# Kernel optimization log

Hardware: AMD Instinct MI355X
Metric: run time of the kernel (lower is better)

The kernel has to match this reference:

```python
import jax, jax.numpy as jnp
import numpy as np

N = 100_000   # nodes
E = 1_600_000 # edges
F = 32        # input features
G = 512       # graphs in batch
EPS = 1e-5    # batchnorm eps


def setup_inputs() -> dict:
    key = jax.random.key(0)
    ks = jax.random.split(key, 24)
    d = {
        "x": jax.random.normal(ks[0], (N, F), jnp.float32),
        "edge_index": jax.random.randint(ks[1], (2, E), 0, N),
        "batch": jnp.sort(jax.random.randint(ks[2], (N,), 0, G)),
        "Wl1": jax.random.normal(ks[3], (30, F), jnp.float32) * 0.1,
        "bl1": jax.random.normal(ks[4], (30,), jnp.float32) * 0.1,
        "Wr1": jax.random.normal(ks[5], (30, F), jnp.float32) * 0.1,
        "Wl2": jax.random.normal(ks[6], (30, 30), jnp.float32) * 0.1,
        "bl2": jax.random.normal(ks[7], (30,), jnp.float32) * 0.1,
        "Wr2": jax.random.normal(ks[8], (30, 30), jnp.float32) * 0.1,
        "g1": jax.random.uniform(ks[9], (30,), jnp.float32) + 0.5,
        "b1": jax.random.normal(ks[10], (30,), jnp.float32) * 0.1,
        "m1": jax.random.normal(ks[11], (30,), jnp.float32) * 0.1,
        "v1": jax.random.uniform(ks[12], (30,), jnp.float32) + 0.5,
        "g2": jax.random.uniform(ks[13], (30,), jnp.float32) + 0.5,
        "b2": jax.random.normal(ks[14], (30,), jnp.float32) * 0.1,
        "m2": jax.random.normal(ks[15], (30,), jnp.float32) * 0.1,
        "v2": jax.random.uniform(ks[16], (30,), jnp.float32) + 0.5,
        "W1": jax.random.normal(ks[17], (10, 60), jnp.float32) * 0.1,
        "bb1": jax.random.normal(ks[18], (10,), jnp.float32) * 0.1,
        "W2": jax.random.normal(ks[19], (1, 10), jnp.float32) * 0.1,
        "bb2": jax.random.normal(ks[20], (1,), jnp.float32) * 0.1,
    }
    return d


def reference(x, edge_index, batch, Wl1, bl1, Wr1, Wl2, bl2, Wr2,
              g1, b1, m1, v1, g2, b2, m2, v2, W1, bb1, W2, bb2):
    src, dst = edge_index[0], edge_index[1]

    def sage(h, Wl, bl, Wr):
        # mean aggregation of source features into targets (PyG SAGEConv default)
        s = jax.ops.segment_sum(h[src], dst, num_segments=N)
        cnt = jax.ops.segment_sum(jnp.ones((E,), h.dtype), dst, num_segments=N)
        agg = s / jnp.maximum(cnt, 1.0)[:, None]
        return agg @ Wl.T + bl + h @ Wr.T

    def bn(h, g, b, m, v):  # BatchNorm1d, eval mode (running stats)
        return (h - m) * jax.lax.rsqrt(v + EPS) * g + b

    h = bn(jax.nn.relu(sage(x, Wl1, bl1, Wr1)), g1, b1, m1, v1)
    h = bn(jax.nn.relu(sage(h, Wl2, bl2, Wr2)), g2, b2, m2, v2)

    # dual segment pooling over graphs
    xmax = jax.ops.segment_max(h, batch, num_segments=G)
    xmax = jnp.where(jnp.isfinite(xmax), xmax, 0.0)  # empty graphs -> 0
    s = jax.ops.segment_sum(h, batch, num_segments=G)
    c = jax.ops.segment_sum(jnp.ones((N,), h.dtype), batch, num_segments=G)
    xmean = s / jnp.maximum(c, 1.0)[:, None]

    z = jnp.concatenate([xmax, xmean], axis=1)  # [G, 60]
    z = jax.nn.relu(z @ W1.T + bb1)
    z = z @ W2.T + bb2
    return jax.nn.sigmoid(z)  # [G, 1]
```

## Files before the change

kernel.cpp:

```cpp
#include <hip/hip_runtime.h>
#include <hip/hip_fp16.h>

#define NN 100000
#define NE 1600000
#define FI 32
#define FH 30
#define PAD 32
#define NG 512
#define NBK 782
#define BNODES 128
#define SCB 1024
#define CBLK 32
#define NCHUNK (SCB / CBLK)
#define CAP 4096
#define NB1 391
#define THB 6250

__global__ __launch_bounds__(256) void k_phist(const int* __restrict__ dst, int* __restrict__ partial,
                                               const float* __restrict__ x, __half2* __restrict__ xh)
{
    __shared__ int cnt[NBK];
    if (blockIdx.x >= SCB) {
        int i = (blockIdx.x - SCB) * 256 + threadIdx.x;
        if (i < NN * (PAD / 2)) {
            float2 f = ((const float2*)x)[i];
            xh[i] = __floats2half2_rn(f.x, f.y);
        }
        return;
    }
    for (int i = threadIdx.x; i < NBK; i += 256) cnt[i] = 0;
    __syncthreads();
    for (int e = blockIdx.x * 256 + threadIdx.x; e < NE; e += SCB * 256)
        atomicAdd(&cnt[dst[e] >> 7], 1);
    __syncthreads();
    for (int i = threadIdx.x; i < NBK; i += 256)
        partial[(size_t)blockIdx.x * NBK + i] = cnt[i];
}

__global__ __launch_bounds__(256) void k_csum(const int* __restrict__ partial, int* __restrict__ chunksum)
{
    int t = blockIdx.x * 256 + threadIdx.x;
    if (t >= NCHUNK * NBK) return;
    int c = t / NBK, b = t - c * NBK;
    int s = 0;
    #pragma unroll 8
    for (int k = 0; k < CBLK; ++k)
        s += partial[(size_t)(c * CBLK + k) * NBK + b];
    chunksum[c * NBK + b] = s;
}

__global__ __launch_bounds__(1024) void k_cscan(const int* __restrict__ chunksum,
                                                int* __restrict__ chunkbase, int* __restrict__ bktOff)
{
    __shared__ int tmp[1024];
    int tid = threadIdx.x;
    int cs[NCHUNK];
    int total = 0;
    if (tid < NBK) {
        #pragma unroll
        for (int c = 0; c < NCHUNK; ++c) { cs[c] = chunksum[c * NBK + tid]; total += cs[c]; }
    }
    tmp[tid] = (tid < NBK) ? total : 0;
    __syncthreads();
    for (int off = 1; off < 1024; off <<= 1) {
        int t = (tid >= off) ? tmp[tid - off] : 0;
        __syncthreads();
        tmp[tid] += t;
        __syncthreads();
    }
    if (tid < NBK) {
        int run = tmp[tid] - total;
        bktOff[tid] = run;
        #pragma unroll
        for (int c = 0; c < NCHUNK; ++c) { chunkbase[c * NBK + tid] = run; run += cs[c]; }
    }
    if (tid == 0) bktOff[NBK] = NE;
}

__global__ __launch_bounds__(256) void k_base(int* __restrict__ partial, const int* __restrict__ chunkbase)
{
    int t = blockIdx.x * 256 + threadIdx.x;
    if (t >= NCHUNK * NBK) return;
    int c = t / NBK, b = t - c * NBK;
    int run = chunkbase[c * NBK + b];
    #pragma unroll 8
    for (int k = 0; k < CBLK; ++k) {
        size_t idx = (size_t)(c * CBLK + k) * NBK + b;
        int v = partial[idx];
        partial[idx] = run;
        run += v;
    }
}

__global__ __launch_bounds__(256) void k_bscat(const int* __restrict__ src, const int* __restrict__ dst,
                                               const int* __restrict__ partial, unsigned* __restrict__ pairs)
{
    __shared__ int sbase[NBK];
    __shared__ int scnt[NBK];
    for (int i = threadIdx.x; i < NBK; i += 256) {
        sbase[i] = partial[(size_t)blockIdx.x * NBK + i];
        scnt[i] = 0;
    }
    __syncthreads();
    for (int e = blockIdx.x * 256 + threadIdx.x; e < NE; e += SCB * 256) {
        int d = dst[e];
        int b = d >> 7;
        int r = atomicAdd(&scnt[b], 1);
        pairs[sbase[b] + r] = ((unsigned)src[e] << 7) | (unsigned)(d & 127);
    }
}

__global__ __launch_bounds__(256) void k_csr(
    const int* __restrict__ bktOff, const unsigned* __restrict__ pairs,
    int* __restrict__ rowstart, int* __restrict__ col)
{
    __shared__ unsigned sp[CAP];
    __shared__ int bins[BNODES], binpos[BNODES], stmp[BNODES];
    int tid = threadIdx.x;
    int bkt = blockIdx.x;
    int gbase = bktOff[bkt];
    int cnt = bktOff[bkt + 1] - gbase;
    if (tid < BNODES) bins[tid] = 0;
    __syncthreads();
    bool inl = (cnt <= CAP);
    if (inl) {
        for (int i = tid; i < cnt; i += 256) {
            unsigned u = pairs[gbase + i];
            sp[i] = u;
            atomicAdd(&bins[u & 127], 1);
        }
    } else {
        for (int i = tid; i < cnt; i += 256)
            atomicAdd(&bins[pairs[gbase + i] & 127], 1);
    }
    __syncthreads();
    if (tid < BNODES) stmp[tid] = bins[tid];
    __syncthreads();
    for (int off = 1; off < BNODES; off <<= 1) {
        int t = 0;
        if (tid < BNODES && tid >= off) t = stmp[tid - off];
        __syncthreads();
        if (tid < BNODES) stmp[tid] += t;
        __syncthreads();
    }
    if (tid < BNODES) {
        int ex = stmp[tid] - bins[tid];
        binpos[tid] = ex;
        int n = (bkt << 7) + tid;
        if (n < NN) rowstart[n] = gbase + ex;
        if (bkt == 0 && tid == 0) rowstart[NN] = NE;
    }
    __syncthreads();
    if (inl) {
        for (int i = tid; i < cnt; i += 256) {
            unsigned u = sp[i];
            int p = atomicAdd(&binpos[u & 127], 1);
            col[gbase + p] = (int)(u >> 7);
        }
    } else {
        for (int i = tid; i < cnt; i += 256) {
            unsigned u = pairs[gbase + i];
            int p = atomicAdd(&binpos[u & 127], 1);
            col[gbase + p] = (int)(u >> 7);
        }
    }
}

__global__ __launch_bounds__(256) void k_aggcsr_h(const int* __restrict__ rowstart,
                                                  const int* __restrict__ col,
                                                  const uint4* __restrict__ hin,
                                                  float* __restrict__ aggout)
{
    int tid = blockIdx.x * 256 + threadIdx.x;
    int n = tid >> 6;
    if (n >= NN) return;
    int lane = threadIdx.x & 63;
    int q = lane & 3;
    int grp = lane >> 2;
    int rs = rowstart[n], re = rowstart[n + 1];
    float a0 = 0.0f, a1 = 0.0f, a2 = 0.0f, a3 = 0.0f;
    float a4 = 0.0f, a5 = 0.0f, a6 = 0.0f, a7 = 0.0f;
    for (int e = rs + grp; e < re; e += 16) {
        uint4 u = hin[(size_t)col[e] * 4 + q];
        float2 f0 = __half22float2(*(const __half2*)&u.x);
        float2 f1 = __half22float2(*(const __half2*)&u.y);
        float2 f2 = __half22float2(*(const __half2*)&u.z);
        float2 f3 = __half22float2(*(const __half2*)&u.w);
        a0 += f0.x; a1 += f0.y; a2 += f1.x; a3 += f1.y;
        a4 += f2.x; a5 += f2.y; a6 += f3.x; a7 += f3.y;
    }
    #pragma unroll
    for (int off = 4; off < 64; off <<= 1) {
        a0 += __shfl_xor(a0, off); a1 += __shfl_xor(a1, off);
        a2 += __shfl_xor(a2, off); a3 += __shfl_xor(a3, off);
        a4 += __shfl_xor(a4, off); a5 += __shfl_xor(a5, off);
        a6 += __shfl_xor(a6, off); a7 += __shfl_xor(a7, off);
    }
    if (lane < 4) {
        float inv = (re > rs) ? 1.0f / (float)(re - rs) : 0.0f;
        float4* o = (float4*)(aggout + (size_t)n * PAD + q * 8);
        o[0] = make_float4(a0 * inv, a1 * inv, a2 * inv, a3 * inv);
        o[1] = make_float4(a4 * inv, a5 * inv, a6 * inv, a7 * inv);
    }
}

__global__ __launch_bounds__(256) void k_t1(
    const float* __restrict__ x, const float* __restrict__ agg,
    const float* __restrict__ Wl, const float* __restrict__ bl, const float* __restrict__ Wr,
    const float* __restrict__ g, const float* __restrict__ b,
    const float* __restrict__ m, const float* __restrict__ v,
    __half2* __restrict__ h1h)
{
    __shared__ float sWl[FH * FI], sWr[FH * FI], sBias[FH], sScale[FH], sShift[FH];
    for (int i = threadIdx.x; i < FH * FI; i += 256) { sWl[i] = Wl[i]; sWr[i] = Wr[i]; }
    if (threadIdx.x < FH) {
        int j = threadIdx.x;
        float sc = g[j] * rsqrtf(v[j] + 1e-5f);
        sBias[j] = bl[j];
        sScale[j] = sc;
        sShift[j] = b[j] - m[j] * sc;
    }
    __syncthreads();
    int n = blockIdx.x * 256 + threadIdx.x;
    if (n >= NN) return;
    float xr[FI], ar[FI];
    #pragma unroll
    for (int k = 0; k < FI; k += 4) {
        float4 xv = *(const float4*)(x + (size_t)n * FI + k);
        float4 av = *(const float4*)(agg + (size_t)n * PAD + k);
        xr[k] = xv.x; xr[k+1] = xv.y; xr[k+2] = xv.z; xr[k+3] = xv.w;
        ar[k] = av.x; ar[k+1] = av.y; ar[k+2] = av.z; ar[k+3] = av.w;
    }
    float res[FH];
    for (int j = 0; j < FH; ++j) {
        float acc = sBias[j];
        #pragma unroll
        for (int k = 0; k < FI; ++k)
            acc += ar[k] * sWl[j * FI + k] + xr[k] * sWr[j * FI + k];
        acc = fmaxf(acc, 0.0f);
        res[j] = acc * sScale[j] + sShift[j];
    }
    __half2* row = h1h + (size_t)n * (PAD / 2);
    #pragma unroll
    for (int j = 0; j < FH; j += 2)
        row[j >> 1] = __floats2half2_rn(res[j], res[j + 1]);
    row[15] = __floats2half2_rn(0.0f, 0.0f);
}

__global__ __launch_bounds__(256) void k_t2(
    const __half2* __restrict__ h1h, const float* __restrict__ agg,
    const float* __restrict__ Wl, const float* __restrict__ bl, const float* __restrict__ Wr,
    const float* __restrict__ g, const float* __restrict__ b,
    const float* __restrict__ m, const float* __restrict__ v,
    __half2* __restrict__ h2h)
{
    __shared__ float sWl[FH * FH], sWr[FH * FH], sBias[FH], sScale[FH], sShift[FH];
    for (int i = threadIdx.x; i < FH * FH; i += 256) { sWl[i] = Wl[i]; sWr[i] = Wr[i]; }
    if (threadIdx.x < FH) {
        int j = threadIdx.x;
        float sc = g[j] * rsqrtf(v[j] + 1e-5f);
        sBias[j] = bl[j];
        sScale[j] = sc;
        sShift[j] = b[j] - m[j] * sc;
    }
    __syncthreads();
    int n = blockIdx.x * 256 + threadIdx.x;
    if (n >= NN) return;
    float xr[FH], ar[FH];
    const __half2* hrow = h1h + (size_t)n * (PAD / 2);
    #pragma unroll
    for (int k2 = 0; k2 < FH / 2; ++k2) {
        float2 fv = __half22float2(hrow[k2]);
        xr[2 * k2] = fv.x; xr[2 * k2 + 1] = fv.y;
    }
    #pragma unroll
    for (int k = 0; k < FH; ++k)
        ar[k] = agg[(size_t)n * PAD + k];
    float res[FH];
    for (int j = 0; j < FH; ++j) {
        float acc = sBias[j];
        #pragma unroll
        for (int k = 0; k < FH; ++k)
            acc += ar[k] * sWl[j * FH + k] + xr[k] * sWr[j * FH + k];
        acc = fmaxf(acc, 0.0f);
        res[j] = acc * sScale[j] + sShift[j];
    }
    __half2* row = h2h + (size_t)n * (PAD / 2);
    #pragma unroll
    for (int j = 0; j < FH; j += 2)
        row[j >> 1] = __floats2half2_rn(res[j], res[j + 1]);
    row[15] = __floats2half2_rn(0.0f, 0.0f);
}

__global__ __launch_bounds__(256) void k_pool(
    const __half* __restrict__ h2, const int* __restrict__ batch,
    const float* __restrict__ W1, const float* __restrict__ bb1,
    const float* __restrict__ W2, const float* __restrict__ bb2,
    float* __restrict__ out)
{
    __shared__ float sS[8][FH], sM[8][FH], sz[2 * FH], st[10];
    int tid = threadIdx.x;
    int gi = blockIdx.x;
    int lo = 0, hi = NN;
    while (lo < hi) { int mid = (lo + hi) >> 1; if (batch[mid] < gi) lo = mid + 1; else hi = mid; }
    int start = lo;
    hi = NN;
    while (lo < hi) { int mid = (lo + hi) >> 1; if (batch[mid] <= gi) lo = mid + 1; else hi = mid; }
    int end = lo;

    int f = tid & 31;
    int ng = tid >> 5;
    float sum = 0.0f, mx = -INFINITY;
    if (f < FH) {
        for (int n = start + ng; n < end; n += 8) {
            float val = __half2float(h2[(size_t)n * PAD + f]);
            sum += val;
            mx = fmaxf(mx, val);
        }
        sS[ng][f] = sum;
        sM[ng][f] = mx;
    }
    __syncthreads();
    if (tid < FH) {
        float s = 0.0f, mm = -INFINITY;
        #pragma unroll
        for (int w = 0; w < 8; ++w) { s += sS[w][tid]; mm = fmaxf(mm, sM[w][tid]); }
        int c = end - start;
        sz[tid]      = (c > 0) ? mm : 0.0f;
        sz[FH + tid] = (c > 0) ? s / (float)c : 0.0f;
    }
    __syncthreads();
    if (tid < 10) {
        float t = bb1[tid];
        for (int k = 0; k < 2 * FH; ++k) t += sz[k] * W1[tid * 2 * FH + k];
        st[tid] = fmaxf(t, 0.0f);
    }
    __syncthreads();
    if (tid == 0) {
        float o = bb2[0];
        for (int j = 0; j < 10; ++j) o += st[j] * W2[j];
        out[gi] = 1.0f / (1.0f + expf(-o));
    }
}

extern "C" void kernel_launch(void* const* d_in, const int* in_sizes, int n_in,
                              void* d_out, int out_size, void* d_ws, size_t ws_size,
                              hipStream_t stream)
{
    const float* x   = (const float*)d_in[0];
    const int*   ei  = (const int*)d_in[1];
    const int*   bat = (const int*)d_in[2];
    const float* Wl1 = (const float*)d_in[3];
    const float* bl1 = (const float*)d_in[4];
    const float* Wr1 = (const float*)d_in[5];
    const float* Wl2 = (const float*)d_in[6];
    const float* bl2 = (const float*)d_in[7];
    const float* Wr2 = (const float*)d_in[8];
    const float* g1  = (const float*)d_in[9];
    const float* b1  = (const float*)d_in[10];
    const float* m1  = (const float*)d_in[11];
    const float* v1  = (const float*)d_in[12];
    const float* g2  = (const float*)d_in[13];
    const float* b2  = (const float*)d_in[14];
    const float* m2  = (const float*)d_in[15];
    const float* v2  = (const float*)d_in[16];
    const float* W1  = (const float*)d_in[17];
    const float* bb1 = (const float*)d_in[18];
    const float* W2  = (const float*)d_in[19];
    const float* bb2 = (const float*)d_in[20];

    const int* src = ei;
    const int* dst = ei + NE;

    int* wsi = (int*)d_ws;
    int*      partial   = wsi;
    int*      chunksum  = partial + (size_t)SCB * NBK;
    int*      chunkbase = chunksum + NCHUNK * NBK;
    int*      bktOff    = chunkbase + NCHUNK * NBK;
    int*      rowstart  = bktOff + NBK + 2;
    unsigned* pairs     = (unsigned*)(rowstart + NN + 4);
    int*      col       = (int*)(pairs + NE);
    __half2*  xh        = (__half2*)(col + NE);
    __half2*  h1h       = xh + (size_t)NN * (PAD / 2);
    __half2*  h2h       = h1h + (size_t)NN * (PAD / 2);
    float*    aggbuf    = (float*)(h2h + (size_t)NN * (PAD / 2));

    int pb = (NCHUNK * NBK + 255) / 256;

    k_phist <<<SCB + THB, 256, 0, stream>>>(dst, partial, x, xh);
    k_csum  <<<pb, 256, 0, stream>>>(partial, chunksum);
    k_cscan <<<1, 1024, 0, stream>>>(chunksum, chunkbase, bktOff);
    k_base  <<<pb, 256, 0, stream>>>(partial, chunkbase);
    k_bscat <<<SCB, 256, 0, stream>>>(src, dst, partial, pairs);
    k_csr   <<<NBK, 256, 0, stream>>>(bktOff, pairs, rowstart, col);

    int ab = (NN * 64 + 255) / 256;
    k_aggcsr_h<<<ab, 256, 0, stream>>>(rowstart, col, (const uint4*)xh, aggbuf);
    k_t1<<<NB1, 256, 0, stream>>>(x, aggbuf, Wl1, bl1, Wr1, g1, b1, m1, v1, h1h);
    k_aggcsr_h<<<ab, 256, 0, stream>>>(rowstart, col, (const uint4*)h1h, aggbuf);
    k_t2<<<NB1, 256, 0, stream>>>(h1h, aggbuf, Wl2, bl2, Wr2, g2, b2, m2, v2, h2h);
    k_pool<<<NG, 256, 0, stream>>>((const __half*)h2h, bat, W1, bb1, W2, bb2, (float*)d_out);
}
```

Measured before the change: 193.4 us.

## Gather node features in FP8 and shrink histogram partials to 16-bit

Node features for both aggregation passes are now stored as packed FP8 (32 bytes per row), so each gathered row is two 16-byte loads instead of four. Each wavefront processes 32 edges per iteration instead of 16, and the aggregation kernel is rewritten around this layout. Separately, the per-block bucket histogram partials become 16-bit, holding only offsets within a bucket, with the global bucket offset added in the scatter kernel; this halves the scan traffic. FP8 storage loses a lot of precision on x and h1 and risks exceeding the accuracy tolerance.

```diff
diff --git a/kernel.cpp b/kernel.cpp
--- a/kernel.cpp
+++ b/kernel.cpp
@@ -14,17 +14,21 @@
 #define NCHUNK (SCB / CBLK)
 #define CAP 4096
 #define NB1 391
-#define THB 6250
-
-__global__ __launch_bounds__(256) void k_phist(const int* __restrict__ dst, int* __restrict__ partial,
-                                               const float* __restrict__ x, __half2* __restrict__ xh)
+#define F8B 3125
+
+__global__ __launch_bounds__(256) void k_phist(const int* __restrict__ dst,
+                                               unsigned short* __restrict__ partial,
+                                               const float* __restrict__ x, unsigned* __restrict__ x8)
 {
     __shared__ int cnt[NBK];
     if (blockIdx.x >= SCB) {
         int i = (blockIdx.x - SCB) * 256 + threadIdx.x;
-        if (i < NN * (PAD / 2)) {
-            float2 f = ((const float2*)x)[i];
-            xh[i] = __floats2half2_rn(f.x, f.y);
+        if (i < NN * 8) {
+            float4 f = ((const float4*)x)[i];
+            unsigned w = 0;
+            w = __builtin_amdgcn_cvt_pk_fp8_f32(f.x, f.y, w, false);
+            w = __builtin_amdgcn_cvt_pk_fp8_f32(f.z, f.w, w, true);
+            x8[i] = w;
         }
         return;
     }
@@ -34,10 +38,11 @@
         atomicAdd(&cnt[dst[e] >> 7], 1);
     __syncthreads();
     for (int i = threadIdx.x; i < NBK; i += 256)
-        partial[(size_t)blockIdx.x * NBK + i] = cnt[i];
-}
-
-__global__ __launch_bounds__(256) void k_csum(const int* __restrict__ partial, int* __restrict__ chunksum)
+        partial[(size_t)blockIdx.x * NBK + i] = (unsigned short)cnt[i];
+}
+
+__global__ __launch_bounds__(256) void k_csum(const unsigned short* __restrict__ partial,
+                                              int* __restrict__ chunksum)
 {
     int t = blockIdx.x * 256 + threadIdx.x;
     if (t >= NCHUNK * NBK) return;
@@ -69,15 +74,16 @@
         __syncthreads();
     }
     if (tid < NBK) {
-        int run = tmp[tid] - total;
-        bktOff[tid] = run;
+        bktOff[tid] = tmp[tid] - total;
+        int run = 0;
         #pragma unroll
         for (int c = 0; c < NCHUNK; ++c) { chunkbase[c * NBK + tid] = run; run += cs[c]; }
     }
     if (tid == 0) bktOff[NBK] = NE;
 }
 
-__global__ __launch_bounds__(256) void k_base(int* __restrict__ partial, const int* __restrict__ chunkbase)
+__global__ __launch_bounds__(256) void k_base(unsigned short* __restrict__ partial,
+                                              const int* __restrict__ chunkbase)
 {
     int t = blockIdx.x * 256 + threadIdx.x;
     if (t >= NCHUNK * NBK) return;
@@ -87,18 +93,20 @@
     for (int k = 0; k < CBLK; ++k) {
         size_t idx = (size_t)(c * CBLK + k) * NBK + b;
         int v = partial[idx];
-        partial[idx] = run;
+        partial[idx] = (unsigned short)run;
         run += v;
     }
 }
 
 __global__ __launch_bounds__(256) void k_bscat(const int* __restrict__ src, const int* __restrict__ dst,
-                                               const int* __restrict__ partial, unsigned* __restrict__ pairs)
+                                               const unsigned short* __restrict__ partial,
+                                               const int* __restrict__ bktOff,
+                                               unsigned* __restrict__ pairs)
 {
     __shared__ int sbase[NBK];
     __shared__ int scnt[NBK];
     for (int i = threadIdx.x; i < NBK; i += 256) {
-        sbase[i] = partial[(size_t)blockIdx.x * NBK + i];
+        sbase[i] = bktOff[i] + (int)partial[(size_t)blockIdx.x * NBK + i];
         scnt[i] = 0;
     }
     __syncthreads();
@@ -166,41 +174,48 @@
     }
 }
 
-__global__ __launch_bounds__(256) void k_aggcsr_h(const int* __restrict__ rowstart,
-                                                  const int* __restrict__ col,
-                                                  const uint4* __restrict__ hin,
-                                                  float* __restrict__ aggout)
+__global__ __launch_bounds__(256) void k_agg8(const int* __restrict__ rowstart,
+                                              const int* __restrict__ col,
+                                              const uint4* __restrict__ hin,
+                                              float* __restrict__ aggout)
 {
     int tid = blockIdx.x * 256 + threadIdx.x;
     int n = tid >> 6;
     if (n >= NN) return;
     int lane = threadIdx.x & 63;
-    int q = lane & 3;
-    int grp = lane >> 2;
+    int q = lane & 1;
+    int grp = lane >> 1;
     int rs = rowstart[n], re = rowstart[n + 1];
-    float a0 = 0.0f, a1 = 0.0f, a2 = 0.0f, a3 = 0.0f;
-    float a4 = 0.0f, a5 = 0.0f, a6 = 0.0f, a7 = 0.0f;
-    for (int e = rs + grp; e < re; e += 16) {
-        uint4 u = hin[(size_t)col[e] * 4 + q];
-        float2 f0 = __half22float2(*(const __half2*)&u.x);
-        float2 f1 = __half22float2(*(const __half2*)&u.y);
-        float2 f2 = __half22float2(*(const __half2*)&u.z);
-        float2 f3 = __half22float2(*(const __half2*)&u.w);
-        a0 += f0.x; a1 += f0.y; a2 += f1.x; a3 += f1.y;
-        a4 += f2.x; a5 += f2.y; a6 += f3.x; a7 += f3.y;
-    }
-    #pragma unroll
-    for (int off = 4; off < 64; off <<= 1) {
-        a0 += __shfl_xor(a0, off); a1 += __shfl_xor(a1, off);
-        a2 += __shfl_xor(a2, off); a3 += __shfl_xor(a3, off);
-        a4 += __shfl_xor(a4, off); a5 += __shfl_xor(a5, off);
-        a6 += __shfl_xor(a6, off); a7 += __shfl_xor(a7, off);
-    }
-    if (lane < 4) {
+    float a[16];
+    #pragma unroll
+    for (int i = 0; i < 16; ++i) a[i] = 0.0f;
+    for (int e = rs + grp; e < re; e += 32) {
+        uint4 u = hin[(size_t)col[e] * 2 + q];
+        auto f0 = __builtin_amdgcn_cvt_pk_f32_fp8(u.x, false);
+        auto f1 = __builtin_amdgcn_cvt_pk_f32_fp8(u.x, true);
+        auto f2 = __builtin_amdgcn_cvt_pk_f32_fp8(u.y, false);
+        auto f3 = __builtin_amdgcn_cvt_pk_f32_fp8(u.y, true);
+        auto f4 = __builtin_amdgcn_cvt_pk_f32_fp8(u.z, false);
+        auto f5 = __builtin_amdgcn_cvt_pk_f32_fp8(u.z, true);
+        auto f6 = __builtin_amdgcn_cvt_pk_f32_fp8(u.w, false);
+        auto f7 = __builtin_amdgcn_cvt_pk_f32_fp8(u.w, true);
+        a[0] += f0[0];  a[1] += f0[1];  a[2]  += f1[0]; a[3]  += f1[1];
+        a[4] += f2[0];  a[5] += f2[1];  a[6]  += f3[0]; a[7]  += f3[1];
+        a[8] += f4[0];  a[9] += f4[1];  a[10] += f5[0]; a[11] += f5[1];
+        a[12] += f6[0]; a[13] += f6[1]; a[14] += f7[0]; a[15] += f7[1];
+    }
+    #pragma unroll
+    for (int off = 2; off < 64; off <<= 1) {
+        #pragma unroll
+        for (int i = 0; i < 16; ++i) a[i] += __shfl_xor(a[i], off);
+    }
+    if (lane < 2) {
         float inv = (re > rs) ? 1.0f / (float)(re - rs) : 0.0f;
-        float4* o = (float4*)(aggout + (size_t)n * PAD + q * 8);
-        o[0] = make_float4(a0 * inv, a1 * inv, a2 * inv, a3 * inv);
-        o[1] = make_float4(a4 * inv, a5 * inv, a6 * inv, a7 * inv);
+        float4* o = (float4*)(aggout + (size_t)n * PAD + q * 16);
+        o[0] = make_float4(a[0] * inv,  a[1] * inv,  a[2] * inv,  a[3] * inv);
+        o[1] = make_float4(a[4] * inv,  a[5] * inv,  a[6] * inv,  a[7] * inv);
+        o[2] = make_float4(a[8] * inv,  a[9] * inv,  a[10] * inv, a[11] * inv);
+        o[3] = make_float4(a[12] * inv, a[13] * inv, a[14] * inv, a[15] * inv);
     }
 }
 
@@ -209,7 +224,7 @@
     const float* __restrict__ Wl, const float* __restrict__ bl, const float* __restrict__ Wr,
     const float* __restrict__ g, const float* __restrict__ b,
     const float* __restrict__ m, const float* __restrict__ v,
-    __half2* __restrict__ h1h)
+    unsigned* __restrict__ h1_8)
 {
     __shared__ float sWl[FH * FI], sWr[FH * FI], sBias[FH], sScale[FH], sShift[FH];
     for (int i = threadIdx.x; i < FH * FI; i += 256) { sWl[i] = Wl[i]; sWr[i] = Wr[i]; }
@@ -231,7 +246,7 @@
         xr[k] = xv.x; xr[k+1] = xv.y; xr[k+2] = xv.z; xr[k+3] = xv.w;
         ar[k] = av.x; ar[k+1] = av.y; ar[k+2] = av.z; ar[k+3] = av.w;
     }
-    float res[FH];
+    float res[32];
     for (int j = 0; j < FH; ++j) {
         float acc = sBias[j];
         #pragma unroll
@@ -240,15 +255,19 @@
         acc = fmaxf(acc, 0.0f);
         res[j] = acc * sScale[j] + sShift[j];
     }
-    __half2* row = h1h + (size_t)n * (PAD / 2);
-    #pragma unroll
-    for (int j = 0; j < FH; j += 2)
-        row[j >> 1] = __floats2half2_rn(res[j], res[j + 1]);
-    row[15] = __floats2half2_rn(0.0f, 0.0f);
+    res[30] = 0.0f; res[31] = 0.0f;
+    unsigned* row = h1_8 + (size_t)n * 8;
+    #pragma unroll
+    for (int w = 0; w < 8; ++w) {
+        unsigned pw = 0;
+        pw = __builtin_amdgcn_cvt_pk_fp8_f32(res[4*w],   res[4*w+1], pw, false);
+        pw = __builtin_amdgcn_cvt_pk_fp8_f32(res[4*w+2], res[4*w+3], pw, true);
+        row[w] = pw;
+    }
 }
 
 __global__ __launch_bounds__(256) void k_t2(
-    const __half2* __restrict__ h1h, const float* __restrict__ agg,
+    const unsigned* __restrict__ h1_8, const float* __restrict__ agg,
     const float* __restrict__ Wl, const float* __restrict__ bl, const float* __restrict__ Wr,
     const float* __restrict__ g, const float* __restrict__ b,
     const float* __restrict__ m, const float* __restrict__ v,
@@ -266,12 +285,14 @@
     __syncthreads();
     int n = blockIdx.x * 256 + threadIdx.x;
     if (n >= NN) return;
-    float xr[FH], ar[FH];
-    const __half2* hrow = h1h + (size_t)n * (PAD / 2);
-    #pragma unroll
-    for (int k2 = 0; k2 < FH / 2; ++k2) {
-        float2 fv = __half22float2(hrow[k2]);
-        xr[2 * k2] = fv.x; xr[2 * k2 + 1] = fv.y;
+    float xr[32], ar[FH];
+    const unsigned* hrow = h1_8 + (size_t)n * 8;
+    #pragma unroll
+    for (int w = 0; w < 8; ++w) {
+        unsigned u = hrow[w];
+        auto lo = __builtin_amdgcn_cvt_pk_f32_fp8(u, false);
+        auto hi = __builtin_amdgcn_cvt_pk_f32_fp8(u, true);
+        xr[4*w] = lo[0]; xr[4*w+1] = lo[1]; xr[4*w+2] = hi[0]; xr[4*w+3] = hi[1];
     }
     #pragma unroll
     for (int k = 0; k < FH; ++k)
@@ -289,7 +310,6 @@
     #pragma unroll
     for (int j = 0; j < FH; j += 2)
         row[j >> 1] = __floats2half2_rn(res[j], res[j + 1]);
-    row[15] = __floats2half2_rn(0.0f, 0.0f);
 }
 
 __global__ __launch_bounds__(256) void k_pool(
@@ -372,32 +392,31 @@
     const int* src = ei;
     const int* dst = ei + NE;
 
-    int* wsi = (int*)d_ws;
-    int*      partial   = wsi;
-    int*      chunksum  = partial + (size_t)SCB * NBK;
-    int*      chunkbase = chunksum + NCHUNK * NBK;
-    int*      bktOff    = chunkbase + NCHUNK * NBK;
-    int*      rowstart  = bktOff + NBK + 2;
-    unsigned* pairs     = (unsigned*)(rowstart + NN + 4);
-    int*      col       = (int*)(pairs + NE);
-    __half2*  xh        = (__half2*)(col + NE);
-    __half2*  h1h       = xh + (size_t)NN * (PAD / 2);
-    __half2*  h2h       = h1h + (size_t)NN * (PAD / 2);
-    float*    aggbuf    = (float*)(h2h + (size_t)NN * (PAD / 2));
+    unsigned short* partial = (unsigned short*)d_ws;
+    int* chunksum  = (int*)((char*)d_ws + (size_t)SCB * NBK * 2);
+    int* chunkbase = chunksum + NCHUNK * NBK;
+    int* bktOff    = chunkbase + NCHUNK * NBK;
+    int* rowstart  = bktOff + NBK + 2;
+    unsigned* pairs = (unsigned*)(rowstart + NN + 4);
+    int* col       = (int*)(pairs + NE);
+    unsigned* x8   = (unsigned*)(col + NE);
+    unsigned* h1_8 = x8 + (size_t)NN * 8;
+    __half2*  h2h  = (__half2*)(h1_8 + (size_t)NN * 8);
+    float* aggbuf  = (float*)(h2h + (size_t)NN * (PAD / 2));
 
     int pb = (NCHUNK * NBK + 255) / 256;
 
-    k_phist <<<SCB + THB, 256, 0, stream>>>(dst, partial, x, xh);
+    k_phist <<<SCB + F8B, 256, 0, stream>>>(dst, partial, x, x8);
     k_csum  <<<pb, 256, 0, stream>>>(partial, chunksum);
     k_cscan <<<1, 1024, 0, stream>>>(chunksum, chunkbase, bktOff);
     k_base  <<<pb, 256, 0, stream>>>(partial, chunkbase);
-    k_bscat <<<SCB, 256, 0, stream>>>(src, dst, partial, pairs);
+    k_bscat <<<SCB, 256, 0, stream>>>(src, dst, partial, bktOff, pairs);
     k_csr   <<<NBK, 256, 0, stream>>>(bktOff, pairs, rowstart, col);
 
     int ab = (NN * 64 + 255) / 256;
-    k_aggcsr_h<<<ab, 256, 0, stream>>>(rowstart, col, (const uint4*)xh, aggbuf);
-    k_t1<<<NB1, 256, 0, stream>>>(x, aggbuf, Wl1, bl1, Wr1, g1, b1, m1, v1, h1h);
-    k_aggcsr_h<<<ab, 256, 0, stream>>>(rowstart, col, (const uint4*)h1h, aggbuf);
-    k_t2<<<NB1, 256, 0, stream>>>(h1h, aggbuf, Wl2, bl2, Wr2, g2, b2, m2, v2, h2h);
+    k_agg8<<<ab, 256, 0, stream>>>(rowstart, col, (const uint4*)x8, aggbuf);
+    k_t1<<<NB1, 256, 0, stream>>>(x, aggbuf, Wl1, bl1, Wr1, g1, b1, m1, v1, h1_8);
+    k_agg8<<<ab, 256, 0, stream>>>(rowstart, col, (const uint4*)h1_8, aggbuf);
+    k_t2<<<NB1, 256, 0, stream>>>(h1_8, aggbuf, Wl2, bl2, Wr2, g2, b2, m2, v2, h2h);
     k_pool<<<NG, 256, 0, stream>>>((const __half*)h2h, bat, W1, bb1, W2, bb2, (float*)d_out);
 }
```

New measurement: 283.8 us. 46.7% more time.
